# Optimization experiments

Hardware: AMD Instinct MI355X
Metric: run time of the kernel (lower is better)

## Reference

```python
import jax, jax.numpy as jnp
import numpy as np

B, K, N_ANN, C = 8, 100000, 32, 80
ALPHA, GAMMA = 0.25, 0.5


def setup_inputs() -> dict:
    key = jax.random.key(0)
    k1, k2, k3, k4, k5, k6, k7 = jax.random.split(key, 7)
    classifications = jax.random.uniform(k1, (B, K, C), jnp.float32, 0.01, 0.99)
    regressions = jax.random.normal(k2, (B, K, 4), jnp.float32)
    # anchors: valid boxes (x1,y1,x2,y2) on a ~1024px image
    a_ctr = jax.random.uniform(k3, (1, K, 2), jnp.float32, 32.0, 992.0)
    a_wh = jax.random.uniform(k4, (1, K, 2), jnp.float32, 16.0, 256.0)
    anchors = jnp.concatenate([a_ctr - a_wh / 2, a_ctr + a_wh / 2], axis=-1)
    # GT annotations: (x1,y1,x2,y2,label), all valid (label >= 0)
    g_ctr = jax.random.uniform(k5, (B, N_ANN, 2), jnp.float32, 64.0, 960.0)
    g_wh = jax.random.uniform(k6, (B, N_ANN, 2), jnp.float32, 16.0, 256.0)
    labels = jax.random.randint(k7, (B, N_ANN, 1), 0, C).astype(jnp.float32)
    annotations = jnp.concatenate([g_ctr - g_wh / 2, g_ctr + g_wh / 2, labels], axis=-1)
    return {"classifications": classifications, "regressions": regressions,
            "anchors": anchors, "annotations": annotations}


def _calc_iou(a, b):
    # a: [K,4] anchors, b: [N,4] gt boxes -> IoU [K,N]
    area_b = (b[:, 2] - b[:, 0]) * (b[:, 3] - b[:, 1])
    area_a = (a[:, 2] - a[:, 0]) * (a[:, 3] - a[:, 1])
    iw = jnp.clip(jnp.minimum(a[:, None, 2], b[None, :, 2]) - jnp.maximum(a[:, None, 0], b[None, :, 0]), 0.0)
    ih = jnp.clip(jnp.minimum(a[:, None, 3], b[None, :, 3]) - jnp.maximum(a[:, None, 1], b[None, :, 1]), 0.0)
    inter = iw * ih
    union = jnp.clip(area_a[:, None] + area_b[None, :] - inter, 1e-8)
    return inter / union


def _per_image(classification, regression, annotation, anchor):
    p = jnp.clip(classification, 1e-4, 1.0 - 1e-4)
    valid = annotation[:, 4] >= 0  # label == -1 means padding
    iou = _calc_iou(anchor, annotation[:, :4])                  # [K,N]
    iou = jnp.where(valid[None, :], iou, -1.0)
    iou_max = jnp.max(iou, axis=1)                               # [K]
    iou_argmax = jnp.argmax(iou, axis=1)                         # [K]
    positive = iou_max >= 0.5                                    # [K]
    num_pos = jnp.sum(positive.astype(jnp.float32))

    assigned = annotation[iou_argmax]                            # [K,5]
    onehot = jax.nn.one_hot(assigned[:, 4].astype(jnp.int32), C, dtype=p.dtype)  # [K,C]
    # targets: -1 = ignore, 0 = negative, 1 = matched class
    base = jnp.where(iou_max < 0.4, 0.0, -1.0)[:, None]          # [K,1]
    targets = jnp.where(positive[:, None], onehot, base)         # [K,C]

    is_pos_cls = targets == 1.0
    alpha_factor = jnp.where(is_pos_cls, ALPHA, 1.0 - ALPHA)
    focal_weight = alpha_factor * jnp.where(is_pos_cls, 1.0 - p, p) ** GAMMA
    bce = -(targets * jnp.log(p) + (1.0 - targets) * jnp.log(1.0 - p))
    cls_loss = jnp.where(targets != -1.0, focal_weight * bce, 0.0)
    cls_loss = jnp.sum(cls_loss) / jnp.clip(num_pos, 1.0)

    aw = anchor[:, 2] - anchor[:, 0]
    ah = anchor[:, 3] - anchor[:, 1]
    acx = anchor[:, 0] + 0.5 * aw
    acy = anchor[:, 1] + 0.5 * ah
    gw = jnp.clip(assigned[:, 2] - assigned[:, 0], 1.0)
    gh = jnp.clip(assigned[:, 3] - assigned[:, 1], 1.0)
    gcx = assigned[:, 0] + 0.5 * gw
    gcy = assigned[:, 1] + 0.5 * gh
    t = jnp.stack([(gcx - acx) / aw, (gcy - acy) / ah, jnp.log(gw / aw), jnp.log(gh / ah)], axis=1)
    t = t / jnp.array([0.1, 0.1, 0.2, 0.2], dtype=t.dtype)
    diff = jnp.abs(t - regression)                               # [K,4]
    sl1 = jnp.where(diff <= 1.0 / 9.0, 0.5 * 9.0 * diff * diff, diff - 0.5 / 9.0)
    reg_sum = jnp.sum(jnp.where(positive[:, None], sl1, 0.0))
    reg_loss = jnp.where(num_pos > 0, reg_sum / jnp.clip(num_pos * 4.0, 1.0), 0.0)
    return cls_loss, reg_loss


def reference(classifications, regressions, anchors, annotations):
    anchor = anchors[0]
    cls_losses, reg_losses = jax.vmap(_per_image, in_axes=(0, 0, 0, None))(
        classifications, regressions, annotations, anchor)
    # original returns mean over batch (keepdim); pack both scalars into [2]
    return jnp.stack([jnp.mean(cls_losses), jnp.mean(reg_losses)])
```

## Files before the change

kernel.cpp:

```cpp
#include <hip/hip_runtime.h>
#include <math.h>

#define B_ 8
#define K_ 100000
#define NANN 32
#define C_ 80
#define BLOCK 256
#define CHUNK 256
#define LN2 0.69314718056f

__global__ void zero_ws_kernel(float* ws) {
    int i = threadIdx.x;
    if (i < 3 * B_) ws[i] = 0.0f;
}

__device__ __forceinline__ float fast_log2(float x) {
#if __has_builtin(__builtin_amdgcn_logf)
    return __builtin_amdgcn_logf(x);
#else
    return __log2f(x);
#endif
}
__device__ __forceinline__ float fast_sqrt(float x) {
#if __has_builtin(__builtin_amdgcn_sqrtf)
    return __builtin_amdgcn_sqrtf(x);
#else
    return sqrtf(x);
#endif
}

__launch_bounds__(BLOCK)
__global__ void focal_main(const float* __restrict__ cls,
                           const float* __restrict__ reg,
                           const float* __restrict__ anc,
                           const float* __restrict__ ann,
                           float* __restrict__ ws) {
    const int b     = blockIdx.y;
    const int chunk = blockIdx.x;
    const int tid   = threadIdx.x;

    __shared__ float s_ann[NANN * 5];
    __shared__ float s_m[CHUNK];
    __shared__ float s_red[(BLOCK / 64) * 3];

    if (tid < NANN * 5) s_ann[tid] = ann[b * NANN * 5 + tid];
    __syncthreads();

    const int k0 = chunk * CHUNK;
    const int k  = k0 + tid;

    float reg_acc  = 0.0f;
    float np_acc   = 0.0f;
    float cls_corr = 0.0f;
    float m        = 0.0f;

    if (k < K_) {
        float4 a = *(const float4*)(anc + (size_t)k * 4);
        float aw = a.z - a.x, ah = a.w - a.y;
        float area_a = aw * ah;

        float best = -2.0f;
        int bestj = 0;
        for (int j = 0; j < NANN; ++j) {
            float bx1 = s_ann[j * 5 + 0], by1 = s_ann[j * 5 + 1];
            float bx2 = s_ann[j * 5 + 2], by2 = s_ann[j * 5 + 3];
            float lbl = s_ann[j * 5 + 4];
            float area_b = (bx2 - bx1) * (by2 - by1);
            float iw = fmaxf(fminf(a.z, bx2) - fmaxf(a.x, bx1), 0.0f);
            float ih = fmaxf(fminf(a.w, by2) - fmaxf(a.y, by1), 0.0f);
            float inter = iw * ih;
            float uni = fmaxf(area_a + area_b - inter, 1e-8f);
            float iou = inter / uni;
            if (lbl < 0.0f) iou = -1.0f;
            if (iou > best) { best = iou; bestj = j; }
        }

        if (best >= 0.5f) {
            m = 1.0f;
            np_acc = 1.0f;
            int c = (int)s_ann[bestj * 5 + 4];
            float p  = cls[((size_t)b * K_ + k) * C_ + c];
            float pm = 1.0f - p;
            float pos_term = -0.25f * fast_sqrt(pm) * (fast_log2(p)  * LN2);
            float neg_term = -0.75f * fast_sqrt(p)  * (fast_log2(pm) * LN2);
            cls_corr = pos_term - neg_term;

            float gx1 = s_ann[bestj * 5 + 0], gy1 = s_ann[bestj * 5 + 1];
            float gx2 = s_ann[bestj * 5 + 2], gy2 = s_ann[bestj * 5 + 3];
            float gw = fmaxf(gx2 - gx1, 1.0f);
            float gh = fmaxf(gy2 - gy1, 1.0f);
            float gcx = gx1 + 0.5f * gw, gcy = gy1 + 0.5f * gh;
            float acx = a.x + 0.5f * aw, acy = a.y + 0.5f * ah;
            float4 r = *(const float4*)(reg + ((size_t)b * K_ + k) * 4);
            float t0 = ((gcx - acx) / aw) * 10.0f;
            float t1 = ((gcy - acy) / ah) * 10.0f;
            float t2 = (fast_log2(gw / aw) * LN2) * 5.0f;
            float t3 = (fast_log2(gh / ah) * LN2) * 5.0f;
            float d, s;
            d = fabsf(t0 - r.x); s = (d <= 1.0f/9.0f) ? 4.5f*d*d : d - 0.5f/9.0f; reg_acc += s;
            d = fabsf(t1 - r.y); s = (d <= 1.0f/9.0f) ? 4.5f*d*d : d - 0.5f/9.0f; reg_acc += s;
            d = fabsf(t2 - r.z); s = (d <= 1.0f/9.0f) ? 4.5f*d*d : d - 0.5f/9.0f; reg_acc += s;
            d = fabsf(t3 - r.w); s = (d <= 1.0f/9.0f) ? 4.5f*d*d : d - 0.5f/9.0f; reg_acc += s;
        } else if (best < 0.4f) {
            m = 1.0f;
        }
    }
    s_m[tid] = m;
    __syncthreads();

    const int na  = min(CHUNK, K_ - k0);
    const int nf4 = na * (C_ / 4);
    const float4* __restrict__ cp =
        (const float4*)(cls + ((size_t)b * K_ + (size_t)k0) * C_);

    float a0 = 0.0f, a1 = 0.0f, a2 = 0.0f, a3 = 0.0f;

    if (na == CHUNK) {
        const int NIT = CHUNK * (C_ / 4) / BLOCK;
#pragma unroll 5
        for (int it = 0; it < NIT; ++it) {
            int idx = tid + it * BLOCK;
            int a_l = (idx * 3277) >> 16;
            float mm = s_m[a_l];
            float4 x = cp[idx];
            a0 = fmaf(mm, fast_sqrt(x.x) * fast_log2(1.0f - x.x), a0);
            a1 = fmaf(mm, fast_sqrt(x.y) * fast_log2(1.0f - x.y), a1);
            a2 = fmaf(mm, fast_sqrt(x.z) * fast_log2(1.0f - x.z), a2);
            a3 = fmaf(mm, fast_sqrt(x.w) * fast_log2(1.0f - x.w), a3);
        }
    } else {
        for (int idx = tid; idx < nf4; idx += BLOCK) {
            int a_l = (idx * 3277) >> 16;
            float mm = s_m[a_l];
            float4 x = cp[idx];
            a0 = fmaf(mm, fast_sqrt(x.x) * fast_log2(1.0f - x.x), a0);
            a1 = fmaf(mm, fast_sqrt(x.y) * fast_log2(1.0f - x.y), a1);
            a2 = fmaf(mm, fast_sqrt(x.z) * fast_log2(1.0f - x.z), a2);
            a3 = fmaf(mm, fast_sqrt(x.w) * fast_log2(1.0f - x.w), a3);
        }
    }

    float cls_acc = ((a0 + a1) + (a2 + a3)) * (-0.75f * LN2) + cls_corr;

    float v0 = cls_acc, v1 = reg_acc, v2 = np_acc;
    for (int off = 32; off > 0; off >>= 1) {
        v0 += __shfl_down(v0, off, 64);
        v1 += __shfl_down(v1, off, 64);
        v2 += __shfl_down(v2, off, 64);
    }
    int wave = tid >> 6, lane = tid & 63;
    if (lane == 0) {
        s_red[wave * 3 + 0] = v0;
        s_red[wave * 3 + 1] = v1;
        s_red[wave * 3 + 2] = v2;
    }
    __syncthreads();
    if (tid == 0) {
        float c = 0.0f, rg = 0.0f, np = 0.0f;
        for (int w = 0; w < BLOCK / 64; ++w) {
            c  += s_red[w * 3 + 0];
            rg += s_red[w * 3 + 1];
            np += s_red[w * 3 + 2];
        }
        atomicAdd(&ws[b * 3 + 0], c);
        atomicAdd(&ws[b * 3 + 1], rg);
        atomicAdd(&ws[b * 3 + 2], np);
    }
}

__global__ void finalize_kernel(const float* __restrict__ ws, float* __restrict__ out) {
    if (threadIdx.x == 0) {
        float cs = 0.0f, rs = 0.0f;
        for (int b = 0; b < B_; ++b) {
            float c  = ws[b * 3 + 0];
            float r  = ws[b * 3 + 1];
            float np = ws[b * 3 + 2];
            cs += c / fmaxf(np, 1.0f);
            rs += (np > 0.0f) ? r / fmaxf(np * 4.0f, 1.0f) : 0.0f;
        }
        out[0] = cs / (float)B_;
        out[1] = rs / (float)B_;
    }
}

extern "C" void kernel_launch(void* const* d_in, const int* in_sizes, int n_in,
                              void* d_out, int out_size, void* d_ws, size_t ws_size,
                              hipStream_t stream) {
    const float* cls = (const float*)d_in[0];
    const float* reg = (const float*)d_in[1];
    const float* anc = (const float*)d_in[2];
    const float* ann = (const float*)d_in[3];
    float* out = (float*)d_out;
    float* ws  = (float*)d_ws;

    zero_ws_kernel<<<1, 64, 0, stream>>>(ws);

    dim3 grid((K_ + CHUNK - 1) / CHUNK, B_);
    focal_main<<<grid, BLOCK, 0, stream>>>(cls, reg, anc, ann, ws);

    finalize_kernel<<<1, 64, 0, stream>>>(ws, out);
}
```

Before: 377.0 us.

## Split anchor assignment and classification sweep into separate kernels with grid-stride MLP

The fused kernel is split in two. The first computes the per-anchor assignment and writes a mask to workspace. The second is a persistent grid-stride sweep over the whole classification tensor that issues 8 independent float4 loads per thread to raise memory-level parallelism. This aims to stream the 256MB classification tensor closer to peak bandwidth. In exchange it adds one kernel launch and a mask write and read through global memory, and it needs a larger workspace of about 3.2MB.

```diff
diff --git a/kernel.cpp b/kernel.cpp
--- a/kernel.cpp
+++ b/kernel.cpp
@@ -6,8 +6,9 @@
 #define NANN 32
 #define C_ 80
 #define BLOCK 256
-#define CHUNK 256
 #define LN2 0.69314718056f
+
+#define WS_M_OFF 32
 
 __global__ void zero_ws_kernel(float* ws) {
     int i = threadIdx.x;
@@ -30,24 +31,20 @@
 }
 
 __launch_bounds__(BLOCK)
-__global__ void focal_main(const float* __restrict__ cls,
-                           const float* __restrict__ reg,
-                           const float* __restrict__ anc,
-                           const float* __restrict__ ann,
-                           float* __restrict__ ws) {
-    const int b     = blockIdx.y;
-    const int chunk = blockIdx.x;
-    const int tid   = threadIdx.x;
+__global__ void focal_assign(const float* __restrict__ cls,
+                             const float* __restrict__ reg,
+                             const float* __restrict__ anc,
+                             const float* __restrict__ ann,
+                             float* __restrict__ ws) {
+    const int b   = blockIdx.y;
+    const int tid = threadIdx.x;
+    const int k   = blockIdx.x * BLOCK + tid;
 
     __shared__ float s_ann[NANN * 5];
-    __shared__ float s_m[CHUNK];
     __shared__ float s_red[(BLOCK / 64) * 3];
 
     if (tid < NANN * 5) s_ann[tid] = ann[b * NANN * 5 + tid];
     __syncthreads();
-
-    const int k0 = chunk * CHUNK;
-    const int k  = k0 + tid;
 
     float reg_acc  = 0.0f;
     float np_acc   = 0.0f;
@@ -104,45 +101,11 @@
         } else if (best < 0.4f) {
             m = 1.0f;
         }
-    }
-    s_m[tid] = m;
-    __syncthreads();
-
-    const int na  = min(CHUNK, K_ - k0);
-    const int nf4 = na * (C_ / 4);
-    const float4* __restrict__ cp =
-        (const float4*)(cls + ((size_t)b * K_ + (size_t)k0) * C_);
-
-    float a0 = 0.0f, a1 = 0.0f, a2 = 0.0f, a3 = 0.0f;
-
-    if (na == CHUNK) {
-        const int NIT = CHUNK * (C_ / 4) / BLOCK;
-#pragma unroll 5
-        for (int it = 0; it < NIT; ++it) {
-            int idx = tid + it * BLOCK;
-            int a_l = (idx * 3277) >> 16;
-            float mm = s_m[a_l];
-            float4 x = cp[idx];
-            a0 = fmaf(mm, fast_sqrt(x.x) * fast_log2(1.0f - x.x), a0);
-            a1 = fmaf(mm, fast_sqrt(x.y) * fast_log2(1.0f - x.y), a1);
-            a2 = fmaf(mm, fast_sqrt(x.z) * fast_log2(1.0f - x.z), a2);
-            a3 = fmaf(mm, fast_sqrt(x.w) * fast_log2(1.0f - x.w), a3);
-        }
-    } else {
-        for (int idx = tid; idx < nf4; idx += BLOCK) {
-            int a_l = (idx * 3277) >> 16;
-            float mm = s_m[a_l];
-            float4 x = cp[idx];
-            a0 = fmaf(mm, fast_sqrt(x.x) * fast_log2(1.0f - x.x), a0);
-            a1 = fmaf(mm, fast_sqrt(x.y) * fast_log2(1.0f - x.y), a1);
-            a2 = fmaf(mm, fast_sqrt(x.z) * fast_log2(1.0f - x.z), a2);
-            a3 = fmaf(mm, fast_sqrt(x.w) * fast_log2(1.0f - x.w), a3);
-        }
-    }
-
-    float cls_acc = ((a0 + a1) + (a2 + a3)) * (-0.75f * LN2) + cls_corr;
-
-    float v0 = cls_acc, v1 = reg_acc, v2 = np_acc;
+
+        ws[WS_M_OFF + (size_t)b * K_ + k] = m;
+    }
+
+    float v0 = cls_corr, v1 = reg_acc, v2 = np_acc;
     for (int off = 32; off > 0; off >>= 1) {
         v0 += __shfl_down(v0, off, 64);
         v1 += __shfl_down(v1, off, 64);
@@ -165,6 +128,65 @@
         atomicAdd(&ws[b * 3 + 0], c);
         atomicAdd(&ws[b * 3 + 1], rg);
         atomicAdd(&ws[b * 3 + 2], np);
+    }
+}
+
+#define SWEEP_GX 256
+#define NF4 (K_ * C_ / 4)
+#define MLP 8
+
+__launch_bounds__(BLOCK, 4)
+__global__ void focal_sweep(const float* __restrict__ cls,
+                            const float* __restrict__ ws_m,
+                            float* __restrict__ ws) {
+    const int b   = blockIdx.y;
+    const int tid = threadIdx.x;
+    const unsigned S  = SWEEP_GX * BLOCK;
+    unsigned g = blockIdx.x * BLOCK + tid;
+
+    const float4* __restrict__ cp = (const float4*)(cls + (size_t)b * K_ * C_);
+    const float*  __restrict__ mb = ws_m + (size_t)b * K_;
+
+    float a0 = 0.0f, a1 = 0.0f, a2 = 0.0f, a3 = 0.0f;
+
+    for (; g + (MLP - 1) * S < (unsigned)NF4; g += MLP * S) {
+        float4 x[MLP];
+        float  mm[MLP];
+#pragma unroll
+        for (int i = 0; i < MLP; ++i) {
+            unsigned gi = g + i * S;
+            x[i]  = cp[gi];
+            mm[i] = mb[gi / 20u];
+        }
+#pragma unroll
+        for (int i = 0; i < MLP; ++i) {
+            a0 = fmaf(mm[i], fast_sqrt(x[i].x) * fast_log2(1.0f - x[i].x), a0);
+            a1 = fmaf(mm[i], fast_sqrt(x[i].y) * fast_log2(1.0f - x[i].y), a1);
+            a2 = fmaf(mm[i], fast_sqrt(x[i].z) * fast_log2(1.0f - x[i].z), a2);
+            a3 = fmaf(mm[i], fast_sqrt(x[i].w) * fast_log2(1.0f - x[i].w), a3);
+        }
+    }
+    for (; g < (unsigned)NF4; g += S) {
+        float4 x = cp[g];
+        float mm = mb[g / 20u];
+        a0 = fmaf(mm, fast_sqrt(x.x) * fast_log2(1.0f - x.x), a0);
+        a1 = fmaf(mm, fast_sqrt(x.y) * fast_log2(1.0f - x.y), a1);
+        a2 = fmaf(mm, fast_sqrt(x.z) * fast_log2(1.0f - x.z), a2);
+        a3 = fmaf(mm, fast_sqrt(x.w) * fast_log2(1.0f - x.w), a3);
+    }
+
+    float cls_acc = ((a0 + a1) + (a2 + a3)) * (-0.75f * LN2);
+
+    __shared__ float s_red[BLOCK / 64];
+    for (int off = 32; off > 0; off >>= 1)
+        cls_acc += __shfl_down(cls_acc, off, 64);
+    int wave = tid >> 6, lane = tid & 63;
+    if (lane == 0) s_red[wave] = cls_acc;
+    __syncthreads();
+    if (tid == 0) {
+        float c = 0.0f;
+        for (int w = 0; w < BLOCK / 64; ++w) c += s_red[w];
+        atomicAdd(&ws[b * 3 + 0], c);
     }
 }
 
@@ -195,8 +217,11 @@
 
     zero_ws_kernel<<<1, 64, 0, stream>>>(ws);
 
-    dim3 grid((K_ + CHUNK - 1) / CHUNK, B_);
-    focal_main<<<grid, BLOCK, 0, stream>>>(cls, reg, anc, ann, ws);
+    dim3 g1((K_ + BLOCK - 1) / BLOCK, B_);
+    focal_assign<<<g1, BLOCK, 0, stream>>>(cls, reg, anc, ann, ws);
+
+    dim3 g2(SWEEP_GX, B_);
+    focal_sweep<<<g2, BLOCK, 0, stream>>>(cls, ws + WS_M_OFF, ws);
 
     finalize_kernel<<<1, 64, 0, stream>>>(ws, out);
 }
```

New measurement: 452.7 us. 20.1% more time.
